# Performance work log

Measured on AMD Instinct MI355X. Metric: run time of the kernel, lower is better.

## Reference

```python
import jax, jax.numpy as jnp
import numpy as np

B, C, H, W = 2, 256, 64, 64
HEADS, SR = 8, 4
D = C // HEADS          # head dim = 32
N = H * W               # query length = 4096
EPS = 1e-5


def _conv(x, w, stride=1, pad=0, groups=1, b=None):
    out = jax.lax.conv_general_dilated(
        x, w, (stride, stride), [(pad, pad), (pad, pad)],
        dimension_numbers=('NCHW', 'OIHW', 'NCHW'),
        feature_group_count=groups)
    if b is not None:
        out = out + b[None, :, None, None]
    return out


def _bn(x, p):
    # p: [4, C] = (gamma, beta, running_mean, running_var), eval-mode BN
    g, b, m, v = p[0], p[1], p[2], p[3]
    s = g / jnp.sqrt(v + EPS)
    return (x - m[None, :, None, None]) * s[None, :, None, None] + b[None, :, None, None]


def setup_inputs() -> dict:
    key = jax.random.key(0)
    ks = iter(jax.random.split(key, 32))
    nrm = lambda shape, s=0.05: jax.random.normal(next(ks), shape, jnp.float32) * s
    def bnp():
        return jnp.stack([jnp.ones((C,), jnp.float32), jnp.zeros((C,), jnp.float32),
                          jax.random.normal(next(ks), (C,), jnp.float32) * 0.1,
                          jax.random.uniform(next(ks), (C,), jnp.float32) + 0.5])
    return dict(
        x=jax.random.normal(next(ks), (B, C, H, W), jnp.float32),
        relative_pos_enc=jax.random.normal(next(ks), (B, 2, 64, 64), jnp.float32),
        q_w=nrm((C, C, 1, 1)), q_b=jnp.zeros((C,), jnp.float32),
        kv_w=nrm((2 * C, C, 1, 1)), kv_b=jnp.zeros((2 * C,), jnp.float32),
        sr1_dw_w=nrm((C, 1, SR + 3, SR + 3)), sr1_bn1=bnp(),
        sr1_pw_w=nrm((C, 1, 1, 1), 0.5), sr1_bn2=bnp(),
        sr2_dw_w=nrm((C, 1, SR // 2 + 3, SR // 2 + 3)), sr2_bn1=bnp(),
        sr2_pw_w=nrm((C, 1, 1, 1), 0.5), sr2_bn2=bnp(),
        local_w=nrm((C, 1, 3, 3)), local_b=jnp.zeros((C,), jnp.float32),
    )


def reference(x, relative_pos_enc, q_w, q_b, kv_w, kv_b,
              sr1_dw_w, sr1_bn1, sr1_pw_w, sr1_bn2,
              sr2_dw_w, sr2_bn1, sr2_pw_w, sr2_bn2,
              local_w, local_b):
    scale = D ** -0.5
    # q: 1x1 conv -> [B, heads, N, D]; both branches use the FIRST half of heads
    q = _conv(x, q_w, b=q_b).reshape(B, HEADS, D, N).transpose(0, 1, 3, 2)
    qh = q[:, :HEADS // 2]

    def branch(dw_w, bn1, pw_w, bn2, stride, pad, rpe_slice):
        # SR path: depthwise conv + BN + ReLU, depthwise 1x1 + BN
        y = jax.nn.relu(_bn(_conv(x, dw_w, stride, pad, groups=C), bn1))
        y = _bn(_conv(y, pw_w, groups=C), bn2)
        # local 3x3 depthwise mixing with residual
        y = _conv(y, local_w, pad=1, groups=C, b=local_b) + y
        kv = _conv(y, kv_w, b=kv_b)                # [B, 2C, h', w']
        k, v = jnp.split(kv, 2, axis=1)
        L = 2 * y.shape[2] * y.shape[3]            # channel-fold doubles kv length
        k = k.reshape(B, HEADS // 2, D, L)
        v = v.reshape(B, HEADS // 2, D, L).transpose(0, 1, 3, 2)
        attn = jnp.einsum('bhnd,bhdl->bhnl', qh, k) * scale
        rpe = jax.image.resize(rpe_slice, (B, 1, N, L), method='bicubic')
        attn = jax.nn.softmax(attn + rpe, axis=-1)
        return jnp.einsum('bhnl,bhld->bhnd', attn, v)

    x1 = branch(sr1_dw_w, sr1_bn1, sr1_pw_w, sr1_bn2,
                SR, (SR + 3) // 2, relative_pos_enc[:, 0:1])
    x2 = branch(sr2_dw_w, sr2_bn1, sr2_pw_w, sr2_bn2,
                SR // 2, (SR // 2 + 3) // 2, relative_pos_enc[:, 1:2])
    out = jnp.concatenate([x1, x2], axis=-1)       # [B, heads//2, N, 2D]
    return out.reshape(B, C, H, W)
```

## Files before the change

### kernel.cpp

```cpp
#include <hip/hip_runtime.h>
#include <hip/hip_bf16.h>
#include <math.h>

#define NB 2
#define NC 256
#define HWIN 4096
#define NN 4096
#define ND 32
#define NHH 4
#define EPSV 1e-5f

typedef short short8 __attribute__((ext_vector_type(8)));
typedef float f32x4 __attribute__((ext_vector_type(4)));
typedef unsigned short u16;
typedef unsigned int u32;

#define OFF_T1   0
#define OFF_T2   262144
#define OFF_Q    1310720
#define OFF_KT1  1835008
#define OFF_VT1  1900544
#define OFF_KT2  1966080
#define OFF_VT2  2228224
#define OFF_RCT1 2490368
#define OFF_RCT2 2531328
#define OFF_WT   2695168
#define OFF_QWT  5054464
#define OFF_LWP  5087232

#define QSCALE 0.2550437314857726f
#define LOG2E  1.4426950408889634f

__device__ __forceinline__ u16 f2bf(float x) {
  unsigned u = __float_as_uint(x);
  u += 0x7fffu + ((u >> 16) & 1u);
  return (u16)(u >> 16);
}

__device__ __forceinline__ u32 pk_bf16(float a, float b) {
  __hip_bfloat162 h = __float22bfloat162_rn(make_float2(a, b));
  u32 r; __builtin_memcpy(&r, &h, 4);
  return r;
}

__device__ __forceinline__ float keysw(float t) {
  t = fabsf(t);
  float w;
  if (t < 1.f)       w = ((1.5f*t - 2.5f)*t)*t + 1.f;
  else if (t < 2.f)  w = ((-0.5f*t + 2.5f)*t - 4.f)*t + 2.f;
  else               w = 0.f;
  return w;
}

template<int KS, int STR, int PAD, int OH>
__device__ __forceinline__ void dwconv_body(int idx, const float* __restrict__ x,
    const float* __restrict__ dww, const float* __restrict__ bn1,
    const float* __restrict__ pww, const float* __restrict__ bn2,
    float* __restrict__ tout) {
  const int hw = OH*OH;
  int s = idx % hw; int c = (idx/hw) % NC; int b = idx/(hw*NC);
  int oy = s / OH, ox = s % OH;
  const float* xp = x + (b*NC + c)*HWIN;
  const float* wp = dww + c*KS*KS;
  float acc = 0.f;
  #pragma unroll
  for (int ky = 0; ky < KS; ++ky) {
    int iy = oy*STR - PAD + ky;
    if (iy < 0 || iy >= 64) continue;
    #pragma unroll
    for (int kx = 0; kx < KS; ++kx) {
      int ix = ox*STR - PAD + kx;
      if (ix < 0 || ix >= 64) continue;
      acc += xp[iy*64 + ix] * wp[ky*KS + kx];
    }
  }
  float s1 = bn1[c] * rsqrtf(bn1[3*NC + c] + EPSV);
  float z = (acc - bn1[2*NC + c])*s1 + bn1[NC + c];
  z = fmaxf(z, 0.f);
  float s2 = bn2[c] * rsqrtf(bn2[3*NC + c] + EPSV);
  z = z * (pww[c]*s2) + (bn2[NC + c] - bn2[2*NC + c]*s2);
  tout[((size_t)(b*hw + s))*NC + c] = z;
}

__device__ __forceinline__ void rpe_body(int idx, const float* __restrict__ rpe,
                                         u16* __restrict__ rcT, int L, int ch) {
  int r = idx & 63; int l = (idx >> 6) % L; int b = idx / (64*L);
  float f = ((float)l + 0.5f)*(64.f/(float)L) - 0.5f;
  int i0 = (int)floorf(f) - 1;
  const float* rp = rpe + ((b*2 + ch)*64 + r)*64;
  float v = 0.f, wsum = 0.f;
  #pragma unroll
  for (int j = 0; j < 4; ++j) {
    int i = i0 + j;
    if (i >= 0 && i < 64) {
      float w = keysw(f - (float)i);
      v += w * rp[i]; wsum += w;
    }
  }
  rcT[((size_t)(b*L + l))*80 + 4 + r] = f2bf(v / wsum);
}

__global__ void __launch_bounds__(256) prep_kernel(
    const float* __restrict__ x,
    const float* __restrict__ dw1, const float* __restrict__ bn11,
    const float* __restrict__ pw1, const float* __restrict__ bn12, float* __restrict__ t1,
    const float* __restrict__ dw2, const float* __restrict__ bn21,
    const float* __restrict__ pw2, const float* __restrict__ bn22, float* __restrict__ t2,
    const float* __restrict__ rpe, u16* __restrict__ rct1, u16* __restrict__ rct2,
    const float* __restrict__ kvw, float* __restrict__ wtp,
    const float* __restrict__ qw, float* __restrict__ qwp2,
    const float* __restrict__ lw, float* __restrict__ lwp) {
  int blk = blockIdx.x;
  int t = threadIdx.x;
  if (blk < 512) {
    dwconv_body<7,4,3,16>(blk*256 + t, x, dw1, bn11, pw1, bn12, t1);
  } else if (blk < 2560) {
    dwconv_body<5,2,2,32>((blk-512)*256 + t, x, dw2, bn21, pw2, bn22, t2);
  } else if (blk < 2816) {
    rpe_body((blk-2560)*256 + t, rpe, rct1, 512, 0);
  } else if (blk < 3840) {
    rpe_body((blk-2816)*256 + t, rpe, rct2, 2048, 1);
  } else if (blk < 3968) {
    int idx = (blk-3840)*256 + t;
    float4 vv = *(const float4*)(kvw + (size_t)idx*4);
    int o = idx >> 6, c4 = idx & 63;
    *(float4*)(wtp + ((size_t)(c4*512 + o))*4) = vv;
  } else if (blk < 4000) {
    int idx = (blk-3968)*256 + t;
    float4 vv = *(const float4*)(qw + (size_t)idx*4);
    int oc = idx >> 6, c0 = (idx & 63)*4;
    int ocq = oc >> 2, r = oc & 3;
    qwp2[((size_t)((c0+0)*32 + ocq))*4 + r] = vv.x;
    qwp2[((size_t)((c0+1)*32 + ocq))*4 + r] = vv.y;
    qwp2[((size_t)((c0+2)*32 + ocq))*4 + r] = vv.z;
    qwp2[((size_t)((c0+3)*32 + ocq))*4 + r] = vv.w;
  } else {
    int c = t;
    #pragma unroll
    for (int tp = 0; tp < 9; ++tp) lwp[tp*256 + c] = lw[c*9 + tp];
  }
}

__global__ void __launch_bounds__(256) localkv_kernel(
    const float* __restrict__ t1T, const float* __restrict__ t2T,
    const float* __restrict__ lwp, const float* __restrict__ lb,
    const float* __restrict__ wtp, const float* __restrict__ kvb,
    u16* __restrict__ kt1, u16* __restrict__ vt1,
    u16* __restrict__ kt2, u16* __restrict__ vt2,
    const float* __restrict__ x, const float* __restrict__ qwp2,
    const float* __restrict__ qb, u16* __restrict__ q) {
  __shared__ float sbuf[128*32];
  int blk = blockIdx.x, tid = threadIdx.x;
  if (blk < 640) {
    int kv = blk & 1, ti = blk >> 1;
    const float* tT; u16 *kT, *vT; int OH, hw, b, s0;
    if (ti < 64) { tT = t1T; kT = kt1; vT = vt1; OH = 16; hw = 256;  b = ti >> 5; s0 = (ti & 31)*8; }
    else { int v2 = ti-64; tT = t2T; kT = kt2; vT = vt2; OH = 32; hw = 1024; b = v2 >> 7; s0 = (v2 & 127)*8; }
    int oy = s0 / OH, ox0 = s0 % OH;
    const float* tb = tT + (size_t)b*hw*NC;
    int cl = tid & 63, spg = tid >> 6;
    int c0 = cl*4;
    f32x4 wt9[9];
    #pragma unroll
    for (int tp = 0; tp < 9; ++tp) wt9[tp] = *(const f32x4*)(lwp + tp*256 + c0);
    f32x4 lb4 = *(const f32x4*)(lb + c0);
    #pragma unroll
    for (int i = 0; i < 2; ++i) {
      int sp = spg*2 + i;
      int ox = ox0 + sp;
      f32x4 a = lb4;
      #pragma unroll
      for (int dy = 0; dy < 3; ++dy) {
        int iy = oy + dy - 1;
        if (iy < 0 || iy >= OH) continue;
        #pragma unroll
        for (int dx = 0; dx < 3; ++dx) {
          int ix = ox + dx - 1;
          if (ix < 0 || ix >= OH) continue;
          f32x4 tv = *(const f32x4*)(tb + (size_t)(iy*OH + ix)*NC + c0);
          a += tv * wt9[dy*3 + dx];
        }
      }
      a += *(const f32x4*)(tb + (size_t)(oy*OH + ox)*NC + c0);
      *(f32x4*)(sbuf + sp*NC + c0) = a;
    }
    __syncthreads();
    int ol = tid & 127, sph = tid >> 7;
    int o0i = kv*256 + ol, o1i = o0i + 128;
    float acc0[4], acc1[4];
    float b0 = kvb[o0i], b1 = kvb[o1i];
    #pragma unroll
    for (int i = 0; i < 4; ++i) { acc0[i] = b0; acc1[i] = b1; }
    #pragma unroll 2
    for (int c4 = 0; c4 < 64; ++c4) {
      f32x4 w0 = *(const f32x4*)(wtp + ((size_t)(c4*512 + o0i))*4);
      f32x4 w1 = *(const f32x4*)(wtp + ((size_t)(c4*512 + o1i))*4);
      #pragma unroll
      for (int i = 0; i < 4; ++i) {
        f32x4 y4 = *(const f32x4*)(sbuf + (sph*4 + i)*NC + c4*4);
        #pragma unroll
        for (int j = 0; j < 4; ++j) { acc0[i] += w0[j]*y4[j]; acc1[i] += w1[j]*y4[j]; }
      }
    }
    int L2 = 2*hw;
    #pragma unroll
    for (int k = 0; k < 2; ++k) {
      const float* ap = k ? acc1 : acc0;
      int oo = ol + k*128;
      int hh = oo >> 6, r = oo & 63, d = r >> 1, e = r & 1;
      if (kv == 0) {
        u16* kp = kT + ((size_t)((b*NHH + hh)*L2 + e*hw + s0 + sph*4))*ND + d;
        #pragma unroll
        for (int j = 0; j < 4; ++j) kp[j*ND] = f2bf(ap[j]);
      } else {
        int l0v = e*hw + s0 + sph*4;
        u16* vp = vT + ((size_t)((b*NHH + hh)*(L2/64) + (l0v >> 6))*ND + d)*64 + (l0v & 63);
        #pragma unroll
        for (int j = 0; j < 4; ++j) vp[j] = f2bf(ap[j]);
      }
    }
  } else {
    int qblk = blk - 640;
    int b = qblk >> 7;
    int n0 = (qblk & 127) * 32;
    const float* xb = x + (size_t)b*NC*HWIN + n0;
    int ocq = tid & 31, spg = tid >> 5;
    float acc[4][4];
    #pragma unroll
    for (int k = 0; k < 4; ++k) {
      float bias = qb[ocq*4 + k];
      #pragma unroll
      for (int i = 0; i < 4; ++i) acc[k][i] = bias;
    }
    #pragma unroll
    for (int half = 0; half < 2; ++half) {
      #pragma unroll
      for (int j = 0; j < 4; ++j) {
        int u = tid + 256*j;
        int c = u >> 3, spq = u & 7;
        *(f32x4*)(sbuf + c*32 + spq*4) =
            *(const f32x4*)(xb + (size_t)(half*128 + c)*HWIN + spq*4);
      }
      __syncthreads();
      #pragma unroll 4
      for (int c = 0; c < 128; ++c) {
        int cg = half*128 + c;
        f32x4 w4 = *(const f32x4*)(qwp2 + ((size_t)(cg*32 + ocq))*4);
        f32x4 y4 = *(const f32x4*)(sbuf + c*32 + spg*4);
        #pragma unroll
        for (int k = 0; k < 4; ++k)
          #pragma unroll
          for (int i = 0; i < 4; ++i) acc[k][i] += w4[k]*y4[i];
      }
      __syncthreads();
    }
    #pragma unroll
    for (int k = 0; k < 4; ++k) {
      int oc = ocq*4 + k;
      int h = oc >> 5, d = oc & 31;
      u16* qp = q + (((size_t)(b*NHH + h))*NN + n0 + spg*4)*ND + d;
      #pragma unroll
      for (int i = 0; i < 4; ++i) qp[i*ND] = f2bf(acc[k][i]*QSCALE);
    }
  }
}

__global__ void __launch_bounds__(256) attn_kernel(
    const u16* __restrict__ qbf,
    const u16* __restrict__ kt1, const u16* __restrict__ vt1, const u16* __restrict__ rct1,
    const u16* __restrict__ kt2, const u16* __restrict__ vt2, const u16* __restrict__ rct2,
    float* __restrict__ out) {
  __shared__ u16 kbuf[2][64*32];
  __shared__ u16 vbuf[2][32*64];
  __shared__ u32 pbuf_all[4][16*32];
  int u = blockIdx.x;
  int br, b, hh, rb;
  if (u < 512) { br = 1; b = u >> 8; hh = (u >> 6) & 3; rb = u & 63; }
  else { int v = u - 512; br = 0; b = v >> 8; hh = (v >> 6) & 3; rb = v & 63; }
  int L = br ? 2048 : 512;
  int nt = br ? 32 : 8;
  const u16* kT  = br ? kt2 : kt1;
  const u16* vT  = br ? vt2 : vt1;
  const u16* rcT = br ? rct2 : rct1;
  int tid = threadIdx.x;
  int w = tid >> 6, lane = tid & 63;
  int g = lane >> 4, lo = lane & 15;
  u32* pbuf = pbuf_all[w];
  u16* pbuf16 = (u16*)pbuf;
  int n = rb*64 + w*16 + lo;

  const u16* kbase = kT + (size_t)(b*NHH + hh)*L*ND;
  const u16* vbase = vT + (size_t)(b*NHH + hh)*ND*L;
  const u16* rcTb  = rcT + (size_t)b*L*80;

  short8 qf = *(const short8*)(qbf + (((size_t)(b*NHH + hh))*NN + n)*ND + 8*g);

  float fr = ((float)n + 0.5f)*(1.f/64.f) - 0.5f;
  int ri0 = (int)floorf(fr) - 1;
  int a = (w < 2) ? rb - 2 : rb - 1;
  int rmin = a & ~3;
  float wr4[4]; float wsum = 0.f;
  #pragma unroll
  for (int j = 0; j < 4; ++j) {
    int i = ri0 + j;
    float wv = (i >= 0 && i < 64) ? keysw(fr - (float)i) : 0.f;
    wr4[j] = wv; wsum += wv;
  }
  float invw = LOG2E / wsum;
  float wt8[8];
  #pragma unroll
  for (int s = 0; s < 8; ++s) {
    float acc = 0.f;
    #pragma unroll
    for (int j = 0; j < 4; ++j)
      acc += (ri0 + j - rmin == s) ? wr4[j]*invw : 0.f;
    wt8[s] = acc;
  }
  short8 wtf;
  {
    u32 p0 = pk_bf16(wt8[0], wt8[1]), p1 = pk_bf16(wt8[2], wt8[3]);
    u32 p2 = pk_bf16(wt8[4], wt8[5]), p3 = pk_bf16(wt8[6], wt8[7]);
    uint4 uu = make_uint4(p0, p1, p2, p3);
    wtf = __builtin_bit_cast(short8, uu);
    if (g != 0) wtf = (short8)0;
  }
  const u16* rcrow0 = rcTb + (rmin + 4);

  const f32x4 zero = {0.f, 0.f, 0.f, 0.f};
  float ssum = 0.f;
  f32x4 o0 = zero, o1 = zero;

  int kr_row = tid >> 2, kr_col = (tid & 3)*8;
  int kr_sw  = ((kr_row >> 1) & 3)*8;
  int vr_row = tid >> 3, vr_col = (tid & 7)*8;
  int vr_sw  = (vr_row & 7)*8;
  int ksw = ((lo >> 1) & 3)*8;
  int vsw = (lo & 7)*8;
  int psw4 = (lo & 7)*4;
  int psw8 = (lo & 7)*8;

  auto stageLoad = [&](short8& kr, short8& vr, int l0) {
    kr = *(const short8*)(kbase + (size_t)(l0 + kr_row)*ND + kr_col);
    vr = *(const short8*)(vbase + (size_t)(l0 >> 6)*(ND*64) + vr_row*64 + vr_col);
  };
  auto stageStore = [&](int bi, short8 kr, short8 vr) {
    *(short8*)(kbuf[bi] + kr_row*32 + (kr_col ^ kr_sw)) = kr;
    *(short8*)(vbuf[bi] + vr_row*64 + (vr_col ^ vr_sw)) = vr;
  };
  auto loadRC = [&](uint4 (&rc)[4], int l0) {
    #pragma unroll
    for (int c = 0; c < 4; ++c) {
      const u16* arow = rcrow0 + (size_t)(l0 + 16*c + lo)*80;
      uint2 ra = *(const uint2*)arow;
      uint2 rb2 = *(const uint2*)(arow + 4);
      rc[c] = make_uint4(ra.x, ra.y, rb2.x, rb2.y);
    }
  };

  short8 kr, vr;
  uint4 rcA[4], rcB[4];
  stageLoad(kr, vr, 0);
  loadRC(rcA, 0);
  stageStore(0, kr, vr);

  for (int t = 0; t < nt; ++t) {
    __syncthreads();
    int cur = t & 1;
    const u16* kb = kbuf[cur];
    const u16* vb = vbuf[cur];
    if (t < nt-1) { stageLoad(kr, vr, (t+1)*64); loadRC(rcB, (t+1)*64); }
    __builtin_amdgcn_s_setprio(1);
    f32x4 s4[4];
    #pragma unroll
    for (int c = 0; c < 4; ++c) {
      short8 rcf = __builtin_bit_cast(short8, rcA[c]);
      f32x4 accr = __builtin_amdgcn_mfma_f32_16x16x32_bf16(rcf, wtf, zero, 0, 0, 0);
      short8 kf = *(const short8*)(kb + (16*c + lo)*32 + ((8*g) ^ ksw));
      s4[c] = __builtin_amdgcn_mfma_f32_16x16x32_bf16(kf, qf, accr, 0, 0, 0);
    }
    float psum = 0.f;
    u32 pk[8];
    #pragma unroll
    for (int c = 0; c < 4; ++c) {
      float p0 = __builtin_amdgcn_exp2f(s4[c][0]);
      float p1 = __builtin_amdgcn_exp2f(s4[c][1]);
      float p2 = __builtin_amdgcn_exp2f(s4[c][2]);
      float p3 = __builtin_amdgcn_exp2f(s4[c][3]);
      psum += (p0 + p1) + (p2 + p3);
      pk[2*c]   = pk_bf16(p0, p1);
      pk[2*c+1] = pk_bf16(p2, p3);
    }
    ssum += psum;
    #pragma unroll
    for (int c = 0; c < 4; ++c)
      *(uint2*)(pbuf + lo*32 + ((8*c + 2*g) ^ psw4)) = make_uint2(pk[2*c], pk[2*c+1]);
    short8 pf0 = *(const short8*)(pbuf16 + lo*64 + ((8*g) ^ psw8));
    short8 pf1 = *(const short8*)(pbuf16 + lo*64 + ((32 + 8*g) ^ psw8));
    short8 v00 = *(const short8*)(vb + lo*64 + ((8*g) ^ vsw));
    short8 v01 = *(const short8*)(vb + lo*64 + ((32 + 8*g) ^ vsw));
    short8 v10 = *(const short8*)(vb + (16 + lo)*64 + ((8*g) ^ vsw));
    short8 v11 = *(const short8*)(vb + (16 + lo)*64 + ((32 + 8*g) ^ vsw));
    o0 = __builtin_amdgcn_mfma_f32_16x16x32_bf16(v00, pf0, o0, 0, 0, 0);
    o1 = __builtin_amdgcn_mfma_f32_16x16x32_bf16(v10, pf0, o1, 0, 0, 0);
    o0 = __builtin_amdgcn_mfma_f32_16x16x32_bf16(v01, pf1, o0, 0, 0, 0);
    o1 = __builtin_amdgcn_mfma_f32_16x16x32_bf16(v11, pf1, o1, 0, 0, 0);
    __builtin_amdgcn_s_setprio(0);
    if (t < nt-1) {
      stageStore(cur ^ 1, kr, vr);
      #pragma unroll
      for (int j = 0; j < 4; ++j) rcA[j] = rcB[j];
    }
  }

  ssum += __shfl_xor(ssum, 16, 64);
  ssum += __shfl_xor(ssum, 32, 64);
  float inv = 1.f/ssum;
  f32x4 w0 = o0*inv, w1 = o1*inv;
  float* op = out + ((size_t)((b*NC + hh*64 + rb)*64 + (w*16 + lo)))*64 + (br ? 32 : 0);
  *(f32x4*)(op + 4*g)      = w0;
  *(f32x4*)(op + 16 + 4*g) = w1;
}

extern "C" void kernel_launch(void* const* d_in, const int* in_sizes, int n_in,
                              void* d_out, int out_size, void* d_ws, size_t ws_size,
                              hipStream_t stream) {
  const float* x    = (const float*)d_in[0];
  const float* rpe  = (const float*)d_in[1];
  const float* qw   = (const float*)d_in[2];
  const float* qb   = (const float*)d_in[3];
  const float* kvw  = (const float*)d_in[4];
  const float* kvb  = (const float*)d_in[5];
  const float* dw1  = (const float*)d_in[6];
  const float* bn11 = (const float*)d_in[7];
  const float* pw1  = (const float*)d_in[8];
  const float* bn12 = (const float*)d_in[9];
  const float* dw2  = (const float*)d_in[10];
  const float* bn21 = (const float*)d_in[11];
  const float* pw2  = (const float*)d_in[12];
  const float* bn22 = (const float*)d_in[13];
  const float* lw   = (const float*)d_in[14];
  const float* lb   = (const float*)d_in[15];
  float* out = (float*)d_out;
  float* ws  = (float*)d_ws;

  float* t1   = ws + OFF_T1;
  float* t2   = ws + OFF_T2;
  u16*   q    = (u16*)(ws + OFF_Q);
  u16*   kt1  = (u16*)(ws + OFF_KT1);
  u16*   vt1  = (u16*)(ws + OFF_VT1);
  u16*   kt2  = (u16*)(ws + OFF_KT2);
  u16*   vt2  = (u16*)(ws + OFF_VT2);
  u16*   rct1 = (u16*)(ws + OFF_RCT1);
  u16*   rct2 = (u16*)(ws + OFF_RCT2);
  float* wtp  = ws + OFF_WT;
  float* qwp2 = ws + OFF_QWT;
  float* lwp  = ws + OFF_LWP;

  hipLaunchKernelGGL(prep_kernel, dim3(4001), dim3(256), 0, stream,
                     x, dw1, bn11, pw1, bn12, t1, dw2, bn21, pw2, bn22, t2,
                     rpe, rct1, rct2, kvw, wtp, qw, qwp2, lw, lwp);
  hipLaunchKernelGGL(localkv_kernel, dim3(896), dim3(256), 0, stream,
                     t1, t2, lwp, lb, wtp, kvb, kt1, vt1, kt2, vt2, x, qwp2, qb, q);
  hipLaunchKernelGGL(attn_kernel, dim3(1024), dim3(256), 0, stream,
                     q, kt1, vt1, rct1, kt2, vt2, rct2, out);
}
```

Measured before the change: 170.5 us.

## Move RPE resize into localkv kernel and unroll attention loop by two

The bicubic RPE resampling blocks move from the prep kernel into the localkv kernel. This rebalances work across the launches: prep shrinks and localkv gets more independent blocks to fill the GPU. The attention main loop is unrolled by two with fixed double-buffer indices, removing the per-iteration buffer selection and the rcA/rcB register copy. It assumes nt is even, which holds for 8 and 32.

```diff
diff --git a/kernel.cpp b/kernel.cpp
--- a/kernel.cpp
+++ b/kernel.cpp
@@ -106,7 +106,6 @@
     const float* __restrict__ pw1, const float* __restrict__ bn12, float* __restrict__ t1,
     const float* __restrict__ dw2, const float* __restrict__ bn21,
     const float* __restrict__ pw2, const float* __restrict__ bn22, float* __restrict__ t2,
-    const float* __restrict__ rpe, u16* __restrict__ rct1, u16* __restrict__ rct2,
     const float* __restrict__ kvw, float* __restrict__ wtp,
     const float* __restrict__ qw, float* __restrict__ qwp2,
     const float* __restrict__ lw, float* __restrict__ lwp) {
@@ -116,17 +115,13 @@
     dwconv_body<7,4,3,16>(blk*256 + t, x, dw1, bn11, pw1, bn12, t1);
   } else if (blk < 2560) {
     dwconv_body<5,2,2,32>((blk-512)*256 + t, x, dw2, bn21, pw2, bn22, t2);
-  } else if (blk < 2816) {
-    rpe_body((blk-2560)*256 + t, rpe, rct1, 512, 0);
-  } else if (blk < 3840) {
-    rpe_body((blk-2816)*256 + t, rpe, rct2, 2048, 1);
-  } else if (blk < 3968) {
-    int idx = (blk-3840)*256 + t;
+  } else if (blk < 2688) {
+    int idx = (blk-2560)*256 + t;
     float4 vv = *(const float4*)(kvw + (size_t)idx*4);
     int o = idx >> 6, c4 = idx & 63;
     *(float4*)(wtp + ((size_t)(c4*512 + o))*4) = vv;
-  } else if (blk < 4000) {
-    int idx = (blk-3968)*256 + t;
+  } else if (blk < 2720) {
+    int idx = (blk-2688)*256 + t;
     float4 vv = *(const float4*)(qw + (size_t)idx*4);
     int oc = idx >> 6, c0 = (idx & 63)*4;
     int ocq = oc >> 2, r = oc & 3;
@@ -148,7 +143,8 @@
     u16* __restrict__ kt1, u16* __restrict__ vt1,
     u16* __restrict__ kt2, u16* __restrict__ vt2,
     const float* __restrict__ x, const float* __restrict__ qwp2,
-    const float* __restrict__ qb, u16* __restrict__ q) {
+    const float* __restrict__ qb, u16* __restrict__ q,
+    const float* __restrict__ rpe, u16* __restrict__ rct1, u16* __restrict__ rct2) {
   __shared__ float sbuf[128*32];
   int blk = blockIdx.x, tid = threadIdx.x;
   if (blk < 640) {
@@ -219,7 +215,7 @@
         for (int j = 0; j < 4; ++j) vp[j] = f2bf(ap[j]);
       }
     }
-  } else {
+  } else if (blk < 896) {
     int qblk = blk - 640;
     int b = qblk >> 7;
     int n0 = (qblk & 127) * 32;
@@ -262,6 +258,10 @@
       #pragma unroll
       for (int i = 0; i < 4; ++i) qp[i*ND] = f2bf(acc[k][i]*QSCALE);
     }
+  } else if (blk < 1152) {
+    rpe_body((blk-896)*256 + tid, rpe, rct1, 512, 0);
+  } else {
+    rpe_body((blk-1152)*256 + tid, rpe, rct2, 2048, 1);
   }
 }
 
@@ -343,9 +343,9 @@
     kr = *(const short8*)(kbase + (size_t)(l0 + kr_row)*ND + kr_col);
     vr = *(const short8*)(vbase + (size_t)(l0 >> 6)*(ND*64) + vr_row*64 + vr_col);
   };
-  auto stageStore = [&](int bi, short8 kr, short8 vr) {
-    *(short8*)(kbuf[bi] + kr_row*32 + (kr_col ^ kr_sw)) = kr;
-    *(short8*)(vbuf[bi] + vr_row*64 + (vr_col ^ vr_sw)) = vr;
+  auto stageStore = [&](u16* kb, u16* vb, short8 kr, short8 vr) {
+    *(short8*)(kb + kr_row*32 + (kr_col ^ kr_sw)) = kr;
+    *(short8*)(vb + vr_row*64 + (vr_col ^ vr_sw)) = vr;
   };
   auto loadRC = [&](uint4 (&rc)[4], int l0) {
     #pragma unroll
@@ -356,24 +356,12 @@
       rc[c] = make_uint4(ra.x, ra.y, rb2.x, rb2.y);
     }
   };
-
-  short8 kr, vr;
-  uint4 rcA[4], rcB[4];
-  stageLoad(kr, vr, 0);
-  loadRC(rcA, 0);
-  stageStore(0, kr, vr);
-
-  for (int t = 0; t < nt; ++t) {
-    __syncthreads();
-    int cur = t & 1;
-    const u16* kb = kbuf[cur];
-    const u16* vb = vbuf[cur];
-    if (t < nt-1) { stageLoad(kr, vr, (t+1)*64); loadRC(rcB, (t+1)*64); }
+  auto computeTile = [&](const u16* kb, const u16* vb, uint4 (&rc)[4]) {
     __builtin_amdgcn_s_setprio(1);
     f32x4 s4[4];
     #pragma unroll
     for (int c = 0; c < 4; ++c) {
-      short8 rcf = __builtin_bit_cast(short8, rcA[c]);
+      short8 rcf = __builtin_bit_cast(short8, rc[c]);
       f32x4 accr = __builtin_amdgcn_mfma_f32_16x16x32_bf16(rcf, wtf, zero, 0, 0, 0);
       short8 kf = *(const short8*)(kb + (16*c + lo)*32 + ((8*g) ^ ksw));
       s4[c] = __builtin_amdgcn_mfma_f32_16x16x32_bf16(kf, qf, accr, 0, 0, 0);
@@ -405,11 +393,24 @@
     o0 = __builtin_amdgcn_mfma_f32_16x16x32_bf16(v01, pf1, o0, 0, 0, 0);
     o1 = __builtin_amdgcn_mfma_f32_16x16x32_bf16(v11, pf1, o1, 0, 0, 0);
     __builtin_amdgcn_s_setprio(0);
-    if (t < nt-1) {
-      stageStore(cur ^ 1, kr, vr);
-      #pragma unroll
-      for (int j = 0; j < 4; ++j) rcA[j] = rcB[j];
-    }
+  };
+
+  short8 kr, vr;
+  uint4 rcA[4], rcB[4];
+  stageLoad(kr, vr, 0);
+  loadRC(rcA, 0);
+  stageStore(kbuf[0], vbuf[0], kr, vr);
+
+  for (int t = 0; t < nt; t += 2) {
+    __syncthreads();
+    stageLoad(kr, vr, (t+1)*64);
+    loadRC(rcB, (t+1)*64);
+    computeTile(kbuf[0], vbuf[0], rcA);
+    stageStore(kbuf[1], vbuf[1], kr, vr);
+    __syncthreads();
+    if (t + 2 < nt) { stageLoad(kr, vr, (t+2)*64); loadRC(rcA, (t+2)*64); }
+    computeTile(kbuf[1], vbuf[1], rcB);
+    if (t + 2 < nt) stageStore(kbuf[0], vbuf[0], kr, vr);
   }
 
   ssum += __shfl_xor(ssum, 16, 64);
@@ -456,11 +457,12 @@
   float* qwp2 = ws + OFF_QWT;
   float* lwp  = ws + OFF_LWP;
 
-  hipLaunchKernelGGL(prep_kernel, dim3(4001), dim3(256), 0, stream,
+  hipLaunchKernelGGL(prep_kernel, dim3(2721), dim3(256), 0, stream,
                      x, dw1, bn11, pw1, bn12, t1, dw2, bn21, pw2, bn22, t2,
-                     rpe, rct1, rct2, kvw, wtp, qw, qwp2, lw, lwp);
-  hipLaunchKernelGGL(localkv_kernel, dim3(896), dim3(256), 0, stream,
-                     t1, t2, lwp, lb, wtp, kvb, kt1, vt1, kt2, vt2, x, qwp2, qb, q);
+                     kvw, wtp, qw, qwp2, lw, lwp);
+  hipLaunchKernelGGL(localkv_kernel, dim3(2176), dim3(256), 0, stream,
+                     t1, t2, lwp, lb, wtp, kvb, kt1, vt1, kt2, vt2, x, qwp2, qb, q,
+                     rpe, rct1, rct2);
   hipLaunchKernelGGL(attn_kernel, dim3(1024), dim3(256), 0, stream,
                      q, kt1, vt1, rct1, kt2, vt2, rct2, out);
 }
```

Result: no change. 170.7 us (+0.1%).
